# Optimization experiments

Hardware: AMD Instinct MI355X
Metric: run time of the kernel (lower is better)

Reference implementation:

```python
import jax, jax.numpy as jnp
import numpy as np

N_NODES = 100000
N_EDGES = 3200000
N_GRAPHS = 512
DIM = 64
NF = 4
BN_EPS = 1e-5

_PARAM_SHAPES = [
    ("c1_w1", (DIM, NF), "randn"), ("c1_b1", (DIM,), "randn"),
    ("c1_g1", (DIM,), "ones"), ("c1_be1", (DIM,), "zeros"),
    ("c1_w2", (DIM, DIM), "randn"), ("c1_b2", (DIM,), "randn"),
    ("bn1_g", (DIM,), "ones"), ("bn1_b", (DIM,), "zeros"),
    ("c2_w1", (DIM, DIM), "randn"), ("c2_b1", (DIM,), "randn"),
    ("c2_g1", (DIM,), "ones"), ("c2_be1", (DIM,), "zeros"),
    ("c2_w2", (DIM, DIM), "randn"), ("c2_b2", (DIM,), "randn"),
    ("bn2_g", (DIM,), "ones"), ("bn2_b", (DIM,), "zeros"),
    ("fc0_w", (DIM, NF), "randn"), ("fc0_b", (DIM,), "randn"),
    ("fc1_w", (DIM, DIM), "randn"), ("fc1_b", (DIM,), "randn"),
    ("fc2_w", (DIM, DIM), "randn"), ("fc2_b", (DIM,), "randn"),
    ("pi_w", (DIM, DIM), "randn"), ("pi_b", (DIM,), "randn"),
    ("vf_w", (DIM, DIM), "randn"), ("vf_b", (DIM,), "randn"),
]


def setup_inputs() -> dict:
    key = jax.random.key(0)
    ks = jax.random.split(key, 3 + len(_PARAM_SHAPES))
    inp = {
        "x": jax.random.normal(ks[0], (N_NODES, NF), jnp.float32),
        "edge_index": jax.random.randint(ks[1], (2, N_EDGES), 0, N_NODES, dtype=jnp.int64)
        if jax.config.jax_enable_x64 else jax.random.randint(ks[1], (2, N_EDGES), 0, N_NODES).astype(jnp.int32),
        "batch": jnp.sort(jax.random.randint(ks[2], (N_NODES,), 0, N_GRAPHS)).astype(jnp.int32),
    }
    for i, (name, shape, fill) in enumerate(_PARAM_SHAPES):
        k = ks[3 + i]
        if fill == "randn":
            inp[name] = jax.random.normal(k, shape, jnp.float32) * 0.1
        elif fill == "ones":
            inp[name] = jnp.ones(shape, jnp.float32)
        else:
            inp[name] = jnp.zeros(shape, jnp.float32)
    return inp


def _lin(x, w, b):
    return x @ w.T + b


def _bn(x, g, b):  # training-mode batch statistics over node axis
    m = x.mean(axis=0)
    v = x.var(axis=0)
    return (x - m) * jax.lax.rsqrt(v + BN_EPS) * g + b


def _gin_conv(x, src, dst, w1, b1, g1, be1, w2, b2):
    # sum-aggregate neighbor messages (GINConv, eps=0): h = MLP(x + sum_{j in N(i)} x_j)
    agg = jax.ops.segment_sum(x[src], dst, num_segments=x.shape[0])
    h = x + agg
    h = jax.nn.relu(_bn(_lin(h, w1, b1), g1, be1))
    return _lin(h, w2, b2)


def reference(x, edge_index, batch,
              c1_w1, c1_b1, c1_g1, c1_be1, c1_w2, c1_b2, bn1_g, bn1_b,
              c2_w1, c2_b1, c2_g1, c2_be1, c2_w2, c2_b2, bn2_g, bn2_b,
              fc0_w, fc0_b, fc1_w, fc1_b, fc2_w, fc2_b,
              pi_w, pi_b, vf_w, vf_b):
    src, dst = edge_index[0], edge_index[1]
    h1 = jax.nn.relu(_bn(_gin_conv(x, src, dst, c1_w1, c1_b1, c1_g1, c1_be1, c1_w2, c1_b2), bn1_g, bn1_b))
    h2 = jax.nn.relu(_bn(_gin_conv(h1, src, dst, c2_w1, c2_b1, c2_g1, c2_be1, c2_w2, c2_b2), bn2_g, bn2_b))
    pool = lambda h: jax.ops.segment_sum(h, batch, num_segments=N_GRAPHS)  # global_add_pool
    # dropout is eval-mode identity
    out = _lin(pool(x), fc0_w, fc0_b) + _lin(pool(h1), fc1_w, fc1_b) + _lin(pool(h2), fc2_w, fc2_b)
    pi = jax.nn.relu(_lin(out, pi_w, pi_b))
    vf = jax.nn.relu(_lin(out, vf_w, vf_b))
    return (pi, vf)
```

## Files before the change

### kernel.cpp

```cpp
#include <hip/hip_runtime.h>

#define N_NODES 100000
#define N_EDGES 3200000
#define N_GRAPHS 512
#define NBKT 782
#define NBLK 256
#define EPB 12500
#define NSCAN 200192
#define NB_SCAN 782
#define SCAP 6000
#define NCOPY 64
#define STREG (NCOPY * 128)

typedef short bf16x8 __attribute__((ext_vector_type(8)));
typedef float f32x4 __attribute__((ext_vector_type(4)));

__device__ __forceinline__ uint32_t f2bf(float f) {
  uint32_t u = __float_as_uint(f);
  return (u + 0x7fffu + ((u >> 16) & 1u)) >> 16;
}
__device__ __forceinline__ float bflo(uint32_t u) { return __uint_as_float(u << 16); }
__device__ __forceinline__ float bfhi(uint32_t u) { return __uint_as_float(u & 0xffff0000u); }

__global__ __launch_bounds__(256) void k_cnt(const int* __restrict__ dst,
                                             int* __restrict__ cnt)
{
  __shared__ int h[NBKT];
  int t = threadIdx.x, blk = blockIdx.x;
  for (int i = t; i < NBKT; i += 256) h[i] = 0;
  __syncthreads();
  int e0 = blk * EPB;
  for (int i = t; i < EPB; i += 256) atomicAdd(&h[dst[e0 + i] >> 7], 1);
  __syncthreads();
  for (int i = t; i < NBKT; i += 256) cnt[i * NBLK + blk] = h[i];
}

__global__ __launch_bounds__(256) void k_scan1(const int* __restrict__ v,
                                               int* __restrict__ bsum, int n)
{
  __shared__ int s[256];
  int i = blockIdx.x * 256 + threadIdx.x;
  s[threadIdx.x] = i < n ? v[i] : 0;
  __syncthreads();
  for (int off = 128; off > 0; off >>= 1) {
    if (threadIdx.x < off) s[threadIdx.x] += s[threadIdx.x + off];
    __syncthreads();
  }
  if (threadIdx.x == 0) bsum[blockIdx.x] = s[0];
}

__global__ void k_scan2(int* __restrict__ bsum, int nb)
{
  __shared__ int s[1024];
  int t = threadIdx.x;
  int v = t < nb ? bsum[t] : 0;
  s[t] = v;
  __syncthreads();
  for (int off = 1; off < 1024; off <<= 1) {
    int nv = t >= off ? s[t - off] : 0;
    __syncthreads();
    s[t] += nv;
    __syncthreads();
  }
  if (t < nb) bsum[t] = s[t] - v;
}

__global__ __launch_bounds__(256) void k_scanout(const int* __restrict__ v,
    const int* __restrict__ boff, int* __restrict__ out, int n)
{
  __shared__ int s[256];
  int t = threadIdx.x, i = blockIdx.x * 256 + t;
  int x = i < n ? v[i] : 0;
  s[t] = x;
  __syncthreads();
  for (int off = 1; off < 256; off <<= 1) {
    int nv = t >= off ? s[t - off] : 0;
    __syncthreads();
    s[t] += nv;
    __syncthreads();
  }
  if (i < n) out[i] = boff[blockIdx.x] + s[t] - x;
}

__global__ __launch_bounds__(256) void k_bin(const int* __restrict__ src,
    const int* __restrict__ dst, const int* __restrict__ off,
    int2* __restrict__ eb)
{
  __shared__ int base[NBKT];
  __shared__ int cur[NBKT];
  int t = threadIdx.x, blk = blockIdx.x;
  for (int i = t; i < NBKT; i += 256) { base[i] = off[i * NBLK + blk]; cur[i] = 0; }
  __syncthreads();
  int e0 = blk * EPB;
  for (int i = t; i < EPB; i += 256) {
    int e = e0 + i;
    int s = src[e], d = dst[e], b = d >> 7;
    int p = atomicAdd(&cur[b], 1);
    eb[base[b] + p] = make_int2(s, d);
  }
}

__global__ __launch_bounds__(256) void k_sortb(const int2* __restrict__ eb,
    const int* __restrict__ off, int* __restrict__ rowstart,
    int* __restrict__ csr)
{
  int b = blockIdx.x, t = threadIdx.x;
  int start = off[b * NBLK];
  int end = (b == NBKT - 1) ? N_EDGES : off[(b + 1) * NBLK];
  int cnt = end - start;
  __shared__ int2 ebs[SCAP];
  __shared__ int h[128], cur[128];
  bool staged = cnt <= SCAP;
  if (staged) for (int i = t; i < cnt; i += 256) ebs[i] = eb[start + i];
  if (t < 128) h[t] = 0;
  __syncthreads();
  if (staged) {
    for (int i = t; i < cnt; i += 256) atomicAdd(&h[ebs[i].y & 127], 1);
  } else {
    for (int i = t; i < cnt; i += 256) atomicAdd(&h[eb[start + i].y & 127], 1);
  }
  __syncthreads();
  int v = t < 128 ? h[t] : 0;
  for (int o = 1; o < 128; o <<= 1) {
    int nv = (t < 128 && t >= o) ? h[t - o] : 0;
    __syncthreads();
    if (t < 128) h[t] += nv;
    __syncthreads();
  }
  if (t < 128) {
    int ex = h[t] - v;
    int node = b * 128 + t;
    if (node < N_NODES) rowstart[node] = start + ex;
    cur[t] = ex;
  }
  if (b == NBKT - 1 && t == 0) rowstart[N_NODES] = N_EDGES;
  __syncthreads();
  if (staged) {
    for (int i = t; i < cnt; i += 256) {
      int2 e = ebs[i];
      int p = atomicAdd(&cur[e.y & 127], 1);
      csr[start + p] = e.x;
    }
  } else {
    for (int i = t; i < cnt; i += 256) {
      int2 e = eb[start + i];
      int p = atomicAdd(&cur[e.y & 127], 1);
      csr[start + p] = e.x;
    }
  }
}

__global__ __launch_bounds__(256) void k_gstart(const int* __restrict__ batch,
                                                int* __restrict__ gstart, int n)
{
  int i = blockIdx.x * 256 + threadIdx.x;
  if (i >= n) return;
  int b = batch[i];
  if (i == 0) {
    for (int g = 0; g <= b; ++g) gstart[g] = 0;
  } else {
    int p = batch[i - 1];
    for (int g = p + 1; g <= b; ++g) gstart[g] = i;
  }
  if (i == n - 1) {
    for (int g = b + 1; g <= N_GRAPHS; ++g) gstart[g] = n;
  }
}

__global__ __launch_bounds__(256) void k_agglin1(const int* __restrict__ csr,
    const int* __restrict__ rowstart, const float* __restrict__ x,
    const float* __restrict__ w1, const float* __restrict__ b1,
    float* __restrict__ OUT, float* __restrict__ st, int n)
{
  __shared__ float sAgg[8][4];
  __shared__ float rs[4][64], rq[4][64];
  int t = threadIdx.x;
  int hw = t >> 5, lane = t & 31;
  int nd = blockIdx.x * 8 + hw;
  const float4* x4 = reinterpret_cast<const float4*>(x);
  float4 a = make_float4(0.f, 0.f, 0.f, 0.f);
  if (nd < n) {
    int e0 = rowstart[nd], e1 = rowstart[nd + 1];
    for (int e = e0 + lane; e < e1; e += 32) {
      float4 v = x4[csr[e]];
      a.x += v.x; a.y += v.y; a.z += v.z; a.w += v.w;
    }
    if (lane == 0) {
      float4 v = x4[nd];
      a.x += v.x; a.y += v.y; a.z += v.z; a.w += v.w;
    }
  }
  for (int off = 1; off < 32; off <<= 1) {
    a.x += __shfl_xor(a.x, off);
    a.y += __shfl_xor(a.y, off);
    a.z += __shfl_xor(a.z, off);
    a.w += __shfl_xor(a.w, off);
  }
  if (lane == 0) *reinterpret_cast<float4*>(&sAgg[hw][0]) = a;
  __syncthreads();
  int d = t & 63, slot = t >> 6;
  float4 wr = reinterpret_cast<const float4*>(w1)[d];
  float bv = b1[d];
  float lsum = 0.f, lsq = 0.f;
  int base = blockIdx.x * 8;
#pragma unroll
  for (int li = slot; li < 8; li += 4) {
    int nn = base + li;
    if (nn < n) {
      float v = bv + sAgg[li][0] * wr.x + sAgg[li][1] * wr.y
                   + sAgg[li][2] * wr.z + sAgg[li][3] * wr.w;
      OUT[nn * 64 + d] = v;
      lsum += v; lsq += v * v;
    }
  }
  rs[slot][d] = lsum; rq[slot][d] = lsq;
  __syncthreads();
  if (t < 64) {
    int cp = (blockIdx.x & (NCOPY - 1)) * 128;
    atomicAdd(&st[cp + d],      rs[0][d] + rs[1][d] + rs[2][d] + rs[3][d]);
    atomicAdd(&st[cp + 64 + d], rq[0][d] + rq[1][d] + rq[2][d] + rq[3][d]);
  }
}

template <bool WRITE_HB>
__global__ __launch_bounds__(256) void k_hpool(const float* __restrict__ T,
    const float* __restrict__ st, const float* __restrict__ gam,
    const float* __restrict__ bet, float invN, const int* __restrict__ batch,
    uint2* __restrict__ Hb, float* __restrict__ pool)
{
  __shared__ float sm[16][64];
  __shared__ int sb[16];
  __shared__ float s_ss[128];
  int t = threadIdx.x;
  int r = t >> 4, c4 = t & 15;
  int row0 = blockIdx.x * 16;
  if (t < 64) {
    float s = 0.f, q = 0.f;
#pragma unroll 8
    for (int c = 0; c < NCOPY; ++c) {
      s += st[c * 128 + t];
      q += st[c * 128 + 64 + t];
    }
    float mean = s * invN;
    float var  = q * invN - mean * mean;
    float sc   = gam[t] * rsqrtf(var + 1e-5f);
    s_ss[t] = sc;
    s_ss[64 + t] = bet[t] - mean * sc;
  }
  if (t >= 64 && t < 80) sb[t - 64] = batch[row0 + t - 64];
  __syncthreads();
  float4 v = reinterpret_cast<const float4*>(T)[(row0 + r) * 16 + c4];
  int c = c4 * 4;
  v.x = fmaxf(v.x * s_ss[c + 0] + s_ss[64 + c + 0], 0.f);
  v.y = fmaxf(v.y * s_ss[c + 1] + s_ss[64 + c + 1], 0.f);
  v.z = fmaxf(v.z * s_ss[c + 2] + s_ss[64 + c + 2], 0.f);
  v.w = fmaxf(v.w * s_ss[c + 3] + s_ss[64 + c + 3], 0.f);
  if (WRITE_HB) {
    uint2 p;
    p.x = f2bf(v.x) | (f2bf(v.y) << 16);
    p.y = f2bf(v.z) | (f2bf(v.w) << 16);
    Hb[(row0 + r) * 16 + c4] = p;
  }
  *reinterpret_cast<float4*>(&sm[r][c]) = v;
  __syncthreads();
  if (t < 64) {
    int gmin = sb[0], gmax = sb[15];
    for (int g = gmin; g <= gmax; ++g) {
      float s = 0.f;
#pragma unroll
      for (int rr = 0; rr < 16; ++rr) if (sb[rr] == g) s += sm[rr][t];
      atomicAdd(&pool[g * 64 + t], s);
    }
  }
}

__global__ __launch_bounds__(256) void k_agg64b(const int* __restrict__ csr,
    const int* __restrict__ rowstart, const uint32_t* __restrict__ Hb,
    float2* __restrict__ AGG, int n)
{
  int hw = threadIdx.x >> 5, lane = threadIdx.x & 31;
  int nd = blockIdx.x * 8 + hw;
  if (nd >= n) return;
  int e = rowstart[nd], e1 = rowstart[nd + 1];
  float a0 = 0.f, a1 = 0.f;
  for (; e + 4 <= e1; e += 4) {
    int s0 = csr[e], s1 = csr[e + 1], s2 = csr[e + 2], s3 = csr[e + 3];
    uint32_t u0 = Hb[s0 * 32 + lane];
    uint32_t u1 = Hb[s1 * 32 + lane];
    uint32_t u2 = Hb[s2 * 32 + lane];
    uint32_t u3 = Hb[s3 * 32 + lane];
    a0 += bflo(u0) + bflo(u1) + bflo(u2) + bflo(u3);
    a1 += bfhi(u0) + bfhi(u1) + bfhi(u2) + bfhi(u3);
  }
  for (; e < e1; ++e) {
    uint32_t u = Hb[csr[e] * 32 + lane];
    a0 += bflo(u); a1 += bfhi(u);
  }
  AGG[nd * 32 + lane] = make_float2(a0, a1);
}

__global__ __launch_bounds__(64) void k_pool_x(const float* __restrict__ x,
    const int* __restrict__ gstart, float* __restrict__ px)
{
  int g = blockIdx.x;
  int r0 = gstart[g], r1 = gstart[g + 1];
  int f = threadIdx.x & 3, slot = threadIdx.x >> 2;
  float acc = 0.f;
  for (int r = r0 + slot; r < r1; r += 16) acc += x[r * 4 + f];
  __shared__ float red[16][4];
  red[slot][f] = acc;
  __syncthreads();
  if (threadIdx.x < 4) {
    float s = 0.f;
    for (int k = 0; k < 16; ++k) s += red[k][f];
    px[g * 4 + f] = s;
  }
}

template <int MODE>
__global__ __launch_bounds__(256) void k_gemm64(const void* __restrict__ IN1,
    const float* __restrict__ IN2, const float* __restrict__ stIn,
    const float* __restrict__ gam, const float* __restrict__ bet, float invN,
    const float* __restrict__ W, const float* __restrict__ bias,
    float* __restrict__ OUT, float* __restrict__ st, int n)
{
  __shared__ float s_ss[128];
  __shared__ float rs[4][64], rq[4][64];
  int tid = threadIdx.x;
  int wav = tid >> 6, lane = tid & 63;
  int m16 = lane & 15, kb = lane >> 4;
  if (MODE == 0 && tid < 64) {
    float s = 0.f, q = 0.f;
#pragma unroll 8
    for (int c = 0; c < NCOPY; ++c) {
      s += stIn[c * 128 + tid];
      q += stIn[c * 128 + 64 + tid];
    }
    float mean = s * invN;
    float var  = q * invN - mean * mean;
    float sc   = gam[tid] * rsqrtf(var + 1e-5f);
    s_ss[tid] = sc;
    s_ss[64 + tid] = bet[tid] - mean * sc;
  }
  __syncthreads();
  float sc0[8], sh0[8], sc1[8], sh1[8];
  if (MODE == 0) {
#pragma unroll
    for (int e = 0; e < 8; e++) {
      sc0[e] = s_ss[kb * 8 + e];       sh0[e] = s_ss[64 + kb * 8 + e];
      sc1[e] = s_ss[32 + kb * 8 + e];  sh1[e] = s_ss[96 + kb * 8 + e];
    }
  }
  bf16x8 Bf[4][2];
#pragma unroll
  for (int tt = 0; tt < 4; tt++)
#pragma unroll
    for (int kh = 0; kh < 2; kh++) {
      const float* wr = W + (tt * 16 + m16) * 64 + kh * 32 + kb * 8;
      float4 w0 = *reinterpret_cast<const float4*>(wr);
      float4 w1 = *reinterpret_cast<const float4*>(wr + 4);
      bf16x8 f;
      f[0] = (short)f2bf(w0.x); f[1] = (short)f2bf(w0.y);
      f[2] = (short)f2bf(w0.z); f[3] = (short)f2bf(w0.w);
      f[4] = (short)f2bf(w1.x); f[5] = (short)f2bf(w1.y);
      f[6] = (short)f2bf(w1.z); f[7] = (short)f2bf(w1.w);
      Bf[tt][kh] = f;
    }
  float bvt[4];
#pragma unroll
  for (int tt = 0; tt < 4; tt++) bvt[tt] = bias[tt * 16 + m16];
  const float4* in2 = reinterpret_cast<const float4*>(IN2);
  const uint2*  in1 = reinterpret_cast<const uint2*>(IN1);
  float lsum[4] = {0.f, 0.f, 0.f, 0.f}, lsq[4] = {0.f, 0.f, 0.f, 0.f};
  int wid = blockIdx.x * 4 + wav, wstride = gridDim.x * 4;
  int ngroups = n >> 4;
  for (int g = wid; g < ngroups; g += wstride) {
    int rbase = g * 16;
    int arow = rbase + m16;
    float av0[8], av1[8];
    if (MODE == 0) {
      float4 q0 = in2[arow * 16 + kb * 2];
      float4 q1 = in2[arow * 16 + kb * 2 + 1];
      float4 q2 = in2[arow * 16 + 8 + kb * 2];
      float4 q3 = in2[arow * 16 + 8 + kb * 2 + 1];
      float r0[8] = {q0.x, q0.y, q0.z, q0.w, q1.x, q1.y, q1.z, q1.w};
      float r1[8] = {q2.x, q2.y, q2.z, q2.w, q3.x, q3.y, q3.z, q3.w};
#pragma unroll
      for (int e = 0; e < 8; e++) {
        av0[e] = fmaxf(r0[e] * sc0[e] + sh0[e], 0.f);
        av1[e] = fmaxf(r1[e] * sc1[e] + sh1[e], 0.f);
      }
    } else {
      uint2 b0 = in1[arow * 16 + kb * 2];
      uint2 b1 = in1[arow * 16 + kb * 2 + 1];
      uint2 b2 = in1[arow * 16 + 8 + kb * 2];
      uint2 b3 = in1[arow * 16 + 8 + kb * 2 + 1];
      float4 g0 = in2[arow * 16 + kb * 2];
      float4 g1 = in2[arow * 16 + kb * 2 + 1];
      float4 g2 = in2[arow * 16 + 8 + kb * 2];
      float4 g3 = in2[arow * 16 + 8 + kb * 2 + 1];
      av0[0] = bflo(b0.x) + g0.x; av0[1] = bfhi(b0.x) + g0.y;
      av0[2] = bflo(b0.y) + g0.z; av0[3] = bfhi(b0.y) + g0.w;
      av0[4] = bflo(b1.x) + g1.x; av0[5] = bfhi(b1.x) + g1.y;
      av0[6] = bflo(b1.y) + g1.z; av0[7] = bfhi(b1.y) + g1.w;
      av1[0] = bflo(b2.x) + g2.x; av1[1] = bfhi(b2.x) + g2.y;
      av1[2] = bflo(b2.y) + g2.z; av1[3] = bfhi(b2.y) + g2.w;
      av1[4] = bflo(b3.x) + g3.x; av1[5] = bfhi(b3.x) + g3.y;
      av1[6] = bflo(b3.y) + g3.z; av1[7] = bfhi(b3.y) + g3.w;
    }
    bf16x8 A0, A1;
#pragma unroll
    for (int e = 0; e < 8; e++) {
      A0[e] = (short)f2bf(av0[e]);
      A1[e] = (short)f2bf(av1[e]);
    }
    f32x4 acc[4];
#pragma unroll
    for (int tt = 0; tt < 4; tt++) {
      acc[tt][0] = bvt[tt]; acc[tt][1] = bvt[tt];
      acc[tt][2] = bvt[tt]; acc[tt][3] = bvt[tt];
      acc[tt] = __builtin_amdgcn_mfma_f32_16x16x32_bf16(A0, Bf[tt][0], acc[tt], 0, 0, 0);
      acc[tt] = __builtin_amdgcn_mfma_f32_16x16x32_bf16(A1, Bf[tt][1], acc[tt], 0, 0, 0);
    }
#pragma unroll
    for (int tt = 0; tt < 4; tt++)
#pragma unroll
      for (int r = 0; r < 4; r++) {
        int row = rbase + kb * 4 + r;
        float v = acc[tt][r];
        OUT[row * 64 + tt * 16 + m16] = v;
        lsum[tt] += v; lsq[tt] += v * v;
      }
  }
#pragma unroll
  for (int tt = 0; tt < 4; tt++) {
    float s = lsum[tt];
    s += __shfl_xor(s, 16); s += __shfl_xor(s, 32);
    lsum[tt] = s;
    float q = lsq[tt];
    q += __shfl_xor(q, 16); q += __shfl_xor(q, 32);
    lsq[tt] = q;
  }
  if (lane < 16) {
#pragma unroll
    for (int tt = 0; tt < 4; tt++) {
      rs[wav][tt * 16 + lane] = lsum[tt];
      rq[wav][tt * 16 + lane] = lsq[tt];
    }
  }
  __syncthreads();
  if (tid < 64) {
    int cp = (blockIdx.x & (NCOPY - 1)) * 128;
    atomicAdd(&st[cp + tid],      rs[0][tid] + rs[1][tid] + rs[2][tid] + rs[3][tid]);
    atomicAdd(&st[cp + 64 + tid], rq[0][tid] + rq[1][tid] + rq[2][tid] + rq[3][tid]);
  }
}

__global__ __launch_bounds__(64) void k_head(const float* __restrict__ px,
    const float* __restrict__ ph1, const float* __restrict__ ph2,
    const float* __restrict__ fc0w, const float* __restrict__ fc0b,
    const float* __restrict__ fc1w, const float* __restrict__ fc1b,
    const float* __restrict__ fc2w, const float* __restrict__ fc2b,
    const float* __restrict__ piw, const float* __restrict__ pib,
    const float* __restrict__ vfw, const float* __restrict__ vfb,
    float* __restrict__ out)
{
  int g = blockIdx.x, d = threadIdx.x;
  float o = fc0b[d] + fc1b[d] + fc2b[d];
  float4 pxv = reinterpret_cast<const float4*>(px)[g];
  float4 w0 = reinterpret_cast<const float4*>(fc0w)[d];
  o += pxv.x * w0.x + pxv.y * w0.y + pxv.z * w0.z + pxv.w * w0.w;
  const float4* p1 = reinterpret_cast<const float4*>(ph1) + g * 16;
  const float4* w1 = reinterpret_cast<const float4*>(fc1w) + d * 16;
  const float4* p2 = reinterpret_cast<const float4*>(ph2) + g * 16;
  const float4* w2 = reinterpret_cast<const float4*>(fc2w) + d * 16;
#pragma unroll
  for (int k = 0; k < 16; k++) {
    float4 a = p1[k], b = w1[k];
    o += a.x * b.x + a.y * b.y + a.z * b.z + a.w * b.w;
    float4 c = p2[k], e = w2[k];
    o += c.x * e.x + c.y * e.y + c.z * e.z + c.w * e.w;
  }
  __shared__ float so[64];
  so[d] = o;
  __syncthreads();
  float p = pib[d], v = vfb[d];
  const float4* sov = reinterpret_cast<const float4*>(so);
  const float4* wp = reinterpret_cast<const float4*>(piw) + d * 16;
  const float4* wv = reinterpret_cast<const float4*>(vfw) + d * 16;
#pragma unroll
  for (int k = 0; k < 16; k++) {
    float4 a = sov[k], b = wp[k], c = wv[k];
    p += a.x * b.x + a.y * b.y + a.z * b.z + a.w * b.w;
    v += a.x * c.x + a.y * c.y + a.z * c.z + a.w * c.w;
  }
  out[g * 64 + d] = fmaxf(p, 0.f);
  out[N_GRAPHS * 64 + g * 64 + d] = fmaxf(v, 0.f);
}

extern "C" void kernel_launch(void* const* d_in, const int* in_sizes, int n_in,
                              void* d_out, int out_size, void* d_ws, size_t ws_size,
                              hipStream_t stream)
{
  const float* x     = (const float*)d_in[0];
  const int*   ei    = (const int*)d_in[1];
  const int*   batch = (const int*)d_in[2];
  const float* c1_w1 = (const float*)d_in[3];
  const float* c1_b1 = (const float*)d_in[4];
  const float* c1_g1 = (const float*)d_in[5];
  const float* c1_be1= (const float*)d_in[6];
  const float* c1_w2 = (const float*)d_in[7];
  const float* c1_b2 = (const float*)d_in[8];
  const float* bn1_g = (const float*)d_in[9];
  const float* bn1_b = (const float*)d_in[10];
  const float* c2_w1 = (const float*)d_in[11];
  const float* c2_b1 = (const float*)d_in[12];
  const float* c2_g1 = (const float*)d_in[13];
  const float* c2_be1= (const float*)d_in[14];
  const float* c2_w2 = (const float*)d_in[15];
  const float* c2_b2 = (const float*)d_in[16];
  const float* bn2_g = (const float*)d_in[17];
  const float* bn2_b = (const float*)d_in[18];
  const float* fc0_w = (const float*)d_in[19];
  const float* fc0_b = (const float*)d_in[20];
  const float* fc1_w = (const float*)d_in[21];
  const float* fc1_b = (const float*)d_in[22];
  const float* fc2_w = (const float*)d_in[23];
  const float* fc2_b = (const float*)d_in[24];
  const float* pi_w  = (const float*)d_in[25];
  const float* pi_b  = (const float*)d_in[26];
  const float* vf_w  = (const float*)d_in[27];
  const float* vf_b  = (const float*)d_in[28];
  const int* src = ei;
  const int* dst = ei + N_EDGES;

  float* ws = (float*)d_ws;
  float* stats    = ws;
  float* ph1      = ws + 32768;
  float* ph2      = ws + 65536;
  float* px       = ws + 98304;
  int*   gstart   = (int*)(ws + 100352);
  int*   bsum     = (int*)(ws + 100880);
  int*   rowstart = (int*)(ws + 101920);
  float* U        = ws + 201936;
  int*   cnt      = (int*)U;
  int*   off      = (int*)U + 200192;
  uint32_t* Hb    = (uint32_t*)U;
  int*   csr      = (int*)(ws + 3401936);
  float* A        = ws + 6601936;
  int2*  eb       = (int2*)A;

  const float invN = 1.0f / (float)N_NODES;

  hipMemsetAsync(ws, 0, 98304 * sizeof(float), stream);

  k_cnt    <<<NBLK, 256, 0, stream>>>(dst, cnt);
  k_scan1  <<<NB_SCAN, 256, 0, stream>>>(cnt, bsum, NSCAN);
  k_scan2  <<<1, 1024, 0, stream>>>(bsum, NB_SCAN);
  k_scanout<<<NB_SCAN, 256, 0, stream>>>(cnt, bsum, off, NSCAN);
  k_bin    <<<NBLK, 256, 0, stream>>>(src, dst, off, eb);
  k_sortb  <<<NBKT, 256, 0, stream>>>(eb, off, rowstart, csr);
  k_gstart <<<(N_NODES + 255) / 256, 256, 0, stream>>>(batch, gstart, N_NODES);

  k_pool_x<<<N_GRAPHS, 64, 0, stream>>>(x, gstart, px);

  k_agglin1<<<N_NODES / 8, 256, 0, stream>>>(csr, rowstart, x, c1_w1, c1_b1,
                                             A, stats + 0 * STREG, N_NODES);
  k_gemm64<0><<<1563, 256, 0, stream>>>(nullptr, A, stats + 0 * STREG,
      c1_g1, c1_be1, invN, c1_w2, c1_b2, A, stats + 1 * STREG, N_NODES);
  k_hpool<true><<<N_NODES / 16, 256, 0, stream>>>(A, stats + 1 * STREG, bn1_g, bn1_b,
      invN, batch, (uint2*)Hb, ph1);

  k_agg64b<<<(N_NODES + 7) / 8, 256, 0, stream>>>(csr, rowstart, Hb, (float2*)A, N_NODES);
  k_gemm64<2><<<1563, 256, 0, stream>>>(Hb, A, nullptr,
      nullptr, nullptr, 0.f, c2_w1, c2_b1, A, stats + 2 * STREG, N_NODES);
  k_gemm64<0><<<1563, 256, 0, stream>>>(nullptr, A, stats + 2 * STREG,
      c2_g1, c2_be1, invN, c2_w2, c2_b2, A, stats + 3 * STREG, N_NODES);
  k_hpool<false><<<N_NODES / 16, 256, 0, stream>>>(A, stats + 3 * STREG, bn2_g, bn2_b,
      invN, batch, nullptr, ph2);

  k_head<<<N_GRAPHS, 64, 0, stream>>>(px, ph1, ph2, fc0_w, fc0_b, fc1_w, fc1_b,
                                      fc2_w, fc2_b, pi_w, pi_b, vf_w, vf_b, (float*)d_out);
}
```

Measured before the change: 335.5 us.

## Fuse layer-2 neighbor aggregation into the first GEMM and pack binned edges

Replaces the separate bf16 gather-aggregate kernel and the MODE-2 GEMM with one kernel. Each wave aggregates 16 destination rows into shared memory, then adds the self features and runs the MFMA linear layer with BN statistics accumulation. This removes the round trip of the 100000x64 fp32 aggregate through global memory and one launch. Separately, binned edges are packed into one int (17-bit source plus 7-bit local destination) instead of an int2, halving bin/sort traffic. The packing relies on node ids fitting in 17 bits.

```diff
diff --git a/kernel.cpp b/kernel.cpp
--- a/kernel.cpp
+++ b/kernel.cpp
@@ -84,7 +84,7 @@
 
 __global__ __launch_bounds__(256) void k_bin(const int* __restrict__ src,
     const int* __restrict__ dst, const int* __restrict__ off,
-    int2* __restrict__ eb)
+    int* __restrict__ eb)
 {
   __shared__ int base[NBKT];
   __shared__ int cur[NBKT];
@@ -96,11 +96,11 @@
     int e = e0 + i;
     int s = src[e], d = dst[e], b = d >> 7;
     int p = atomicAdd(&cur[b], 1);
-    eb[base[b] + p] = make_int2(s, d);
-  }
-}
-
-__global__ __launch_bounds__(256) void k_sortb(const int2* __restrict__ eb,
+    eb[base[b] + p] = s | ((d & 127) << 17);
+  }
+}
+
+__global__ __launch_bounds__(256) void k_sortb(const int* __restrict__ eb,
     const int* __restrict__ off, int* __restrict__ rowstart,
     int* __restrict__ csr)
 {
@@ -108,16 +108,16 @@
   int start = off[b * NBLK];
   int end = (b == NBKT - 1) ? N_EDGES : off[(b + 1) * NBLK];
   int cnt = end - start;
-  __shared__ int2 ebs[SCAP];
+  __shared__ int ebs[SCAP];
   __shared__ int h[128], cur[128];
   bool staged = cnt <= SCAP;
   if (staged) for (int i = t; i < cnt; i += 256) ebs[i] = eb[start + i];
   if (t < 128) h[t] = 0;
   __syncthreads();
   if (staged) {
-    for (int i = t; i < cnt; i += 256) atomicAdd(&h[ebs[i].y & 127], 1);
+    for (int i = t; i < cnt; i += 256) atomicAdd(&h[(ebs[i] >> 17) & 127], 1);
   } else {
-    for (int i = t; i < cnt; i += 256) atomicAdd(&h[eb[start + i].y & 127], 1);
+    for (int i = t; i < cnt; i += 256) atomicAdd(&h[(eb[start + i] >> 17) & 127], 1);
   }
   __syncthreads();
   int v = t < 128 ? h[t] : 0;
@@ -137,15 +137,15 @@
   __syncthreads();
   if (staged) {
     for (int i = t; i < cnt; i += 256) {
-      int2 e = ebs[i];
-      int p = atomicAdd(&cur[e.y & 127], 1);
-      csr[start + p] = e.x;
+      int e = ebs[i];
+      int p = atomicAdd(&cur[(e >> 17) & 127], 1);
+      csr[start + p] = e & 0x1FFFF;
     }
   } else {
     for (int i = t; i < cnt; i += 256) {
-      int2 e = eb[start + i];
-      int p = atomicAdd(&cur[e.y & 127], 1);
-      csr[start + p] = e.x;
+      int e = eb[start + i];
+      int p = atomicAdd(&cur[(e >> 17) & 127], 1);
+      csr[start + p] = e & 0x1FFFF;
     }
   }
 }
@@ -274,31 +274,6 @@
   }
 }
 
-__global__ __launch_bounds__(256) void k_agg64b(const int* __restrict__ csr,
-    const int* __restrict__ rowstart, const uint32_t* __restrict__ Hb,
-    float2* __restrict__ AGG, int n)
-{
-  int hw = threadIdx.x >> 5, lane = threadIdx.x & 31;
-  int nd = blockIdx.x * 8 + hw;
-  if (nd >= n) return;
-  int e = rowstart[nd], e1 = rowstart[nd + 1];
-  float a0 = 0.f, a1 = 0.f;
-  for (; e + 4 <= e1; e += 4) {
-    int s0 = csr[e], s1 = csr[e + 1], s2 = csr[e + 2], s3 = csr[e + 3];
-    uint32_t u0 = Hb[s0 * 32 + lane];
-    uint32_t u1 = Hb[s1 * 32 + lane];
-    uint32_t u2 = Hb[s2 * 32 + lane];
-    uint32_t u3 = Hb[s3 * 32 + lane];
-    a0 += bflo(u0) + bflo(u1) + bflo(u2) + bflo(u3);
-    a1 += bfhi(u0) + bfhi(u1) + bfhi(u2) + bfhi(u3);
-  }
-  for (; e < e1; ++e) {
-    uint32_t u = Hb[csr[e] * 32 + lane];
-    a0 += bflo(u); a1 += bfhi(u);
-  }
-  AGG[nd * 32 + lane] = make_float2(a0, a1);
-}
-
 __global__ __launch_bounds__(64) void k_pool_x(const float* __restrict__ x,
     const int* __restrict__ gstart, float* __restrict__ px)
 {
@@ -314,6 +289,127 @@
     float s = 0.f;
     for (int k = 0; k < 16; ++k) s += red[k][f];
     px[g * 4 + f] = s;
+  }
+}
+
+__global__ __launch_bounds__(256) void k_aggmm(const int* __restrict__ csr,
+    const int* __restrict__ rowstart, const uint32_t* __restrict__ Hb,
+    const float* __restrict__ W, const float* __restrict__ bias,
+    float* __restrict__ OUT, float* __restrict__ st, int n)
+{
+  __shared__ float sA[4][16][68];
+  __shared__ float rs[4][64], rq[4][64];
+  int tid = threadIdx.x;
+  int wav = tid >> 6, lane = tid & 63;
+  int m16 = lane & 15, kb = lane >> 4;
+  int hw = lane >> 5, lane31 = lane & 31;
+  bf16x8 Bf[4][2];
+#pragma unroll
+  for (int tt = 0; tt < 4; tt++)
+#pragma unroll
+    for (int kh = 0; kh < 2; kh++) {
+      const float* wr = W + (tt * 16 + m16) * 64 + kh * 32 + kb * 8;
+      float4 w0 = *reinterpret_cast<const float4*>(wr);
+      float4 w1 = *reinterpret_cast<const float4*>(wr + 4);
+      bf16x8 f;
+      f[0] = (short)f2bf(w0.x); f[1] = (short)f2bf(w0.y);
+      f[2] = (short)f2bf(w0.z); f[3] = (short)f2bf(w0.w);
+      f[4] = (short)f2bf(w1.x); f[5] = (short)f2bf(w1.y);
+      f[6] = (short)f2bf(w1.z); f[7] = (short)f2bf(w1.w);
+      Bf[tt][kh] = f;
+    }
+  float bvt[4];
+#pragma unroll
+  for (int tt = 0; tt < 4; tt++) bvt[tt] = bias[tt * 16 + m16];
+  int base = blockIdx.x * 64 + wav * 16;
+  if (base < n) {
+#pragma unroll 2
+    for (int i = 0; i < 8; i++) {
+      int nd = base + 2 * i + hw;
+      int e = rowstart[nd], e1 = rowstart[nd + 1];
+      float a0 = 0.f, a1 = 0.f;
+      for (; e + 4 <= e1; e += 4) {
+        int s0 = csr[e], s1 = csr[e + 1], s2 = csr[e + 2], s3 = csr[e + 3];
+        uint32_t u0 = Hb[s0 * 32 + lane31];
+        uint32_t u1 = Hb[s1 * 32 + lane31];
+        uint32_t u2 = Hb[s2 * 32 + lane31];
+        uint32_t u3 = Hb[s3 * 32 + lane31];
+        a0 += bflo(u0) + bflo(u1) + bflo(u2) + bflo(u3);
+        a1 += bfhi(u0) + bfhi(u1) + bfhi(u2) + bfhi(u3);
+      }
+      for (; e < e1; ++e) {
+        uint32_t u = Hb[csr[e] * 32 + lane31];
+        a0 += bflo(u); a1 += bfhi(u);
+      }
+      *reinterpret_cast<float2*>(&sA[wav][2 * i + hw][lane31 * 2]) =
+          make_float2(a0, a1);
+    }
+  }
+  __syncthreads();
+  float lsum[4] = {0.f, 0.f, 0.f, 0.f}, lsq[4] = {0.f, 0.f, 0.f, 0.f};
+  if (base < n) {
+    int arow = base + m16;
+    const uint2* in1 = reinterpret_cast<const uint2*>(Hb);
+    uint2 b0 = in1[arow * 16 + kb * 2];
+    uint2 b1 = in1[arow * 16 + kb * 2 + 1];
+    uint2 b2 = in1[arow * 16 + 8 + kb * 2];
+    uint2 b3 = in1[arow * 16 + 8 + kb * 2 + 1];
+    const float* la0 = &sA[wav][m16][kb * 8];
+    const float* la1 = &sA[wav][m16][32 + kb * 8];
+    float av0[8], av1[8];
+    av0[0] = bflo(b0.x) + la0[0]; av0[1] = bfhi(b0.x) + la0[1];
+    av0[2] = bflo(b0.y) + la0[2]; av0[3] = bfhi(b0.y) + la0[3];
+    av0[4] = bflo(b1.x) + la0[4]; av0[5] = bfhi(b1.x) + la0[5];
+    av0[6] = bflo(b1.y) + la0[6]; av0[7] = bfhi(b1.y) + la0[7];
+    av1[0] = bflo(b2.x) + la1[0]; av1[1] = bfhi(b2.x) + la1[1];
+    av1[2] = bflo(b2.y) + la1[2]; av1[3] = bfhi(b2.y) + la1[3];
+    av1[4] = bflo(b3.x) + la1[4]; av1[5] = bfhi(b3.x) + la1[5];
+    av1[6] = bflo(b3.y) + la1[6]; av1[7] = bfhi(b3.y) + la1[7];
+    bf16x8 A0, A1;
+#pragma unroll
+    for (int e = 0; e < 8; e++) {
+      A0[e] = (short)f2bf(av0[e]);
+      A1[e] = (short)f2bf(av1[e]);
+    }
+    f32x4 acc[4];
+#pragma unroll
+    for (int tt = 0; tt < 4; tt++) {
+      acc[tt][0] = bvt[tt]; acc[tt][1] = bvt[tt];
+      acc[tt][2] = bvt[tt]; acc[tt][3] = bvt[tt];
+      acc[tt] = __builtin_amdgcn_mfma_f32_16x16x32_bf16(A0, Bf[tt][0], acc[tt], 0, 0, 0);
+      acc[tt] = __builtin_amdgcn_mfma_f32_16x16x32_bf16(A1, Bf[tt][1], acc[tt], 0, 0, 0);
+    }
+#pragma unroll
+    for (int tt = 0; tt < 4; tt++)
+#pragma unroll
+      for (int r = 0; r < 4; r++) {
+        int row = base + kb * 4 + r;
+        float v = acc[tt][r];
+        OUT[row * 64 + tt * 16 + m16] = v;
+        lsum[tt] += v; lsq[tt] += v * v;
+      }
+  }
+#pragma unroll
+  for (int tt = 0; tt < 4; tt++) {
+    float s = lsum[tt];
+    s += __shfl_xor(s, 16); s += __shfl_xor(s, 32);
+    lsum[tt] = s;
+    float q = lsq[tt];
+    q += __shfl_xor(q, 16); q += __shfl_xor(q, 32);
+    lsq[tt] = q;
+  }
+  if (lane < 16) {
+#pragma unroll
+    for (int tt = 0; tt < 4; tt++) {
+      rs[wav][tt * 16 + lane] = lsum[tt];
+      rq[wav][tt * 16 + lane] = lsq[tt];
+    }
+  }
+  __syncthreads();
+  if (tid < 64) {
+    int cp = (blockIdx.x & (NCOPY - 1)) * 128;
+    atomicAdd(&st[cp + tid],      rs[0][tid] + rs[1][tid] + rs[2][tid] + rs[3][tid]);
+    atomicAdd(&st[cp + 64 + tid], rq[0][tid] + rq[1][tid] + rq[2][tid] + rq[3][tid]);
   }
 }
 
@@ -370,7 +466,6 @@
 #pragma unroll
   for (int tt = 0; tt < 4; tt++) bvt[tt] = bias[tt * 16 + m16];
   const float4* in2 = reinterpret_cast<const float4*>(IN2);
-  const uint2*  in1 = reinterpret_cast<const uint2*>(IN1);
   float lsum[4] = {0.f, 0.f, 0.f, 0.f}, lsq[4] = {0.f, 0.f, 0.f, 0.f};
   int wid = blockIdx.x * 4 + wav, wstride = gridDim.x * 4;
   int ngroups = n >> 4;
@@ -378,35 +473,16 @@
     int rbase = g * 16;
     int arow = rbase + m16;
     float av0[8], av1[8];
-    if (MODE == 0) {
-      float4 q0 = in2[arow * 16 + kb * 2];
-      float4 q1 = in2[arow * 16 + kb * 2 + 1];
-      float4 q2 = in2[arow * 16 + 8 + kb * 2];
-      float4 q3 = in2[arow * 16 + 8 + kb * 2 + 1];
-      float r0[8] = {q0.x, q0.y, q0.z, q0.w, q1.x, q1.y, q1.z, q1.w};
-      float r1[8] = {q2.x, q2.y, q2.z, q2.w, q3.x, q3.y, q3.z, q3.w};
-#pragma unroll
-      for (int e = 0; e < 8; e++) {
-        av0[e] = fmaxf(r0[e] * sc0[e] + sh0[e], 0.f);
-        av1[e] = fmaxf(r1[e] * sc1[e] + sh1[e], 0.f);
-      }
-    } else {
-      uint2 b0 = in1[arow * 16 + kb * 2];
-      uint2 b1 = in1[arow * 16 + kb * 2 + 1];
-      uint2 b2 = in1[arow * 16 + 8 + kb * 2];
-      uint2 b3 = in1[arow * 16 + 8 + kb * 2 + 1];
-      float4 g0 = in2[arow * 16 + kb * 2];
-      float4 g1 = in2[arow * 16 + kb * 2 + 1];
-      float4 g2 = in2[arow * 16 + 8 + kb * 2];
-      float4 g3 = in2[arow * 16 + 8 + kb * 2 + 1];
-      av0[0] = bflo(b0.x) + g0.x; av0[1] = bfhi(b0.x) + g0.y;
-      av0[2] = bflo(b0.y) + g0.z; av0[3] = bfhi(b0.y) + g0.w;
-      av0[4] = bflo(b1.x) + g1.x; av0[5] = bfhi(b1.x) + g1.y;
-      av0[6] = bflo(b1.y) + g1.z; av0[7] = bfhi(b1.y) + g1.w;
-      av1[0] = bflo(b2.x) + g2.x; av1[1] = bfhi(b2.x) + g2.y;
-      av1[2] = bflo(b2.y) + g2.z; av1[3] = bfhi(b2.y) + g2.w;
-      av1[4] = bflo(b3.x) + g3.x; av1[5] = bfhi(b3.x) + g3.y;
-      av1[6] = bflo(b3.y) + g3.z; av1[7] = bfhi(b3.y) + g3.w;
+    float4 q0 = in2[arow * 16 + kb * 2];
+    float4 q1 = in2[arow * 16 + kb * 2 + 1];
+    float4 q2 = in2[arow * 16 + 8 + kb * 2];
+    float4 q3 = in2[arow * 16 + 8 + kb * 2 + 1];
+    float r0[8] = {q0.x, q0.y, q0.z, q0.w, q1.x, q1.y, q1.z, q1.w};
+    float r1[8] = {q2.x, q2.y, q2.z, q2.w, q3.x, q3.y, q3.z, q3.w};
+#pragma unroll
+    for (int e = 0; e < 8; e++) {
+      av0[e] = fmaxf(r0[e] * sc0[e] + sh0[e], 0.f);
+      av1[e] = fmaxf(r1[e] * sc1[e] + sh1[e], 0.f);
     }
     bf16x8 A0, A1;
 #pragma unroll
@@ -548,7 +624,7 @@
   uint32_t* Hb    = (uint32_t*)U;
   int*   csr      = (int*)(ws + 3401936);
   float* A        = ws + 6601936;
-  int2*  eb       = (int2*)A;
+  int*   eb       = (int*)A;
 
   const float invN = 1.0f / (float)N_NODES;
 
@@ -571,9 +647,8 @@
   k_hpool<true><<<N_NODES / 16, 256, 0, stream>>>(A, stats + 1 * STREG, bn1_g, bn1_b,
       invN, batch, (uint2*)Hb, ph1);
 
-  k_agg64b<<<(N_NODES + 7) / 8, 256, 0, stream>>>(csr, rowstart, Hb, (float2*)A, N_NODES);
-  k_gemm64<2><<<1563, 256, 0, stream>>>(Hb, A, nullptr,
-      nullptr, nullptr, 0.f, c2_w1, c2_b1, A, stats + 2 * STREG, N_NODES);
+  k_aggmm<<<(N_NODES + 63) / 64, 256, 0, stream>>>(csr, rowstart, Hb,
+      c2_w1, c2_b1, A, stats + 2 * STREG, N_NODES);
   k_gemm64<0><<<1563, 256, 0, stream>>>(nullptr, A, stats + 2 * STREG,
       c2_g1, c2_be1, invN, c2_w2, c2_b2, A, stats + 3 * STREG, N_NODES);
   k_hpool<false><<<N_NODES / 16, 256, 0, stream>>>(A, stats + 3 * STREG, bn2_g, bn2_b,
```

After: 360.8 us. 1.08x slower.
